# Kernel tuning notes

Measured on AMD Instinct MI355X. Metric: run time of the kernel, lower is better.

The kernel has to match this reference:

```python
import jax, jax.numpy as jnp
import numpy as np

H = 8          # n_heads
EPS = 1e-5     # LayerNorm eps (torch default)


def setup_inputs() -> dict:
    key = jax.random.key(0)
    ks = jax.random.split(key, 16)
    B, N, D, L, C, K = 2, 1000, 6, 12, 32, 16
    dm = L * C  # d_model = 384
    s = 0.02
    inp = {
        "x": jax.random.normal(ks[0], (B, N, D, L, C), dtype=jnp.float32),
        "topk_index": jax.random.randint(ks[1], (B, N, K), 0, N),
        # attention projections (stored as [in, out]; y = x @ W + b)
        "Wq": jax.random.normal(ks[2], (dm, dm), jnp.float32) * s,
        "bq": jnp.zeros((dm,), jnp.float32),
        "Wk": jax.random.normal(ks[3], (dm, dm), jnp.float32) * s,
        "bk": jnp.zeros((dm,), jnp.float32),
        "Wv": jax.random.normal(ks[4], (dm, dm), jnp.float32) * s,
        "bv": jnp.zeros((dm,), jnp.float32),
        "Wo": jax.random.normal(ks[5], (dm, dm), jnp.float32) * s,
        "bo": jnp.zeros((dm,), jnp.float32),
        # LayerNorm over last dim C
        "ln_g": jnp.ones((C,), jnp.float32),
        "ln_b": jnp.zeros((C,), jnp.float32),
        # MLP: C -> 2C -> C with GELU
        "W1": jax.random.normal(ks[6], (C, 2 * C), jnp.float32) * s,
        "b1": jnp.zeros((2 * C,), jnp.float32),
        "W2": jax.random.normal(ks[7], (2 * C, C), jnp.float32) * s,
        "b2": jnp.zeros((C,), jnp.float32),
    }
    return inp


def _forward(x, topk_index, Wq, bq, Wk, bk, Wv, bv, Wo, bo, ln_g, ln_b, W1, b1, W2, b2):
    B, N, D, L, C = x.shape
    dm = L * C
    dk = dm // H

    q = x.reshape(B * N, D, dm)                                   # [BN, D, dm]
    # gather top-k neighbor features: kv[b,i] = x[b, topk_index[b,i]]
    kv = x[jnp.arange(B)[:, None, None], topk_index]              # [B, N, K, D, L, C]
    K_ = topk_index.shape[-1]
    kv = kv.reshape(B * N, K_ * D, dm)                            # [BN, KD, dm]

    Q = (q @ Wq + bq).reshape(B * N, D, H, dk)
    Kp = (kv @ Wk + bk).reshape(B * N, K_ * D, H, dk)
    V = (kv @ Wv + bv).reshape(B * N, K_ * D, H, dk)

    scale = 1.0 / jnp.sqrt(jnp.asarray(dk, x.dtype))
    scores = jnp.einsum('blhe,bshe->bhls', Q, Kp) * scale         # [BN, H, D, KD]
    A = jax.nn.softmax(scores, axis=-1)                           # dropout: eval mode (identity)
    ctx = jnp.einsum('bhls,bshd->blhd', A, V).reshape(B * N, D, dm)
    ctx = (ctx @ Wo + bo).reshape(B, N, D, L, C)

    h = x + ctx                                                   # residual (dropout = identity)
    mu = jnp.mean(h, axis=-1, keepdims=True)
    var = jnp.var(h, axis=-1, keepdims=True)
    fused = (h - mu) / jnp.sqrt(var + EPS) * ln_g + ln_b          # LayerNorm over C

    mlp = jax.nn.gelu(fused @ W1 + b1, approximate=False) @ W2 + b2
    return fused + mlp


def reference(x, topk_index, Wq, bq, Wk, bk, Wv, bv, Wo, bo, ln_g, ln_b, W1, b1, W2, b2):
    return _forward(x, topk_index, Wq, bq, Wk, bk, Wv, bv, Wo, bo, ln_g, ln_b, W1, b1, W2, b2)
```

## Files before the change

### kernel.cpp

```cpp
#include <hip/hip_runtime.h>

#define NB 2
#define NN 1000
#define ND 6
#define NK 16
#define NH 8
#define DM 384
#define MROWS 12000
#define NTOK 2000
#define NS 96

static __device__ __forceinline__ float4 ld4(const float* p){ return *reinterpret_cast<const float4*>(p); }
static __device__ __forceinline__ void st4(float* p, float4 v){ *reinterpret_cast<float4*>(p) = v; }

#define SCALE 0.14433756729740646f
#define GELU_K 0.70710678118654752f

__global__ __launch_bounds__(256, 2)
void k_qkv(const float* __restrict__ x,
           const float* __restrict__ Wq, const float* __restrict__ bq,
           const float* __restrict__ Wk, const float* __restrict__ bk,
           const float* __restrict__ Wv, const float* __restrict__ bv,
           float* __restrict__ Qa, float* __restrict__ Ka, float* __restrict__ Va)
{
    __shared__ float As[16*132];
    __shared__ float Bs[16*128];

    const int tid = threadIdx.x;
    const int tx = tid & 15, ty = tid >> 4;
    const int r0 = blockIdx.x * 128;
    const int wsel = blockIdx.y / 3;
    const int c0 = (blockIdx.y % 3) * 128;
    const float* W   = (wsel == 0) ? Wq : (wsel == 1) ? Wk : Wv;
    const float* bi  = (wsel == 0) ? bq : (wsel == 1) ? bk : bv;
    float*       out = (wsel == 0) ? Qa : (wsel == 1) ? Ka : Va;

    float acc[8][8];
    #pragma unroll
    for (int i = 0; i < 8; i++)
        #pragma unroll
        for (int j = 0; j < 8; j++) acc[i][j] = 0.f;

    const int lrow = tid >> 2;
    const int lkc  = (tid & 3) << 2;
    const int bkr  = tid >> 5;
    const int bcc  = (tid & 31) << 2;

    for (int k0 = 0; k0 < DM; k0 += 16) {
        #pragma unroll
        for (int hf = 0; hf < 2; hf++) {
            const int r = lrow + hf*64;
            const int gr = r0 + r;
            float4 v = make_float4(0.f, 0.f, 0.f, 0.f);
            if (gr < MROWS) v = ld4(&x[(size_t)gr*DM + k0 + lkc]);
            As[(lkc+0)*132 + r] = v.x;
            As[(lkc+1)*132 + r] = v.y;
            As[(lkc+2)*132 + r] = v.z;
            As[(lkc+3)*132 + r] = v.w;
        }
        #pragma unroll
        for (int hf = 0; hf < 2; hf++) {
            const int kr = bkr + hf*8;
            st4(&Bs[kr*128 + bcc], ld4(&W[(size_t)(k0+kr)*DM + c0 + bcc]));
        }
        __syncthreads();
        #pragma unroll
        for (int kk = 0; kk < 16; kk++) {
            const float4 a0 = ld4(&As[kk*132 + 4*ty]);
            const float4 a1 = ld4(&As[kk*132 + 64 + 4*ty]);
            const float4 b0 = ld4(&Bs[kk*128 + 4*tx]);
            const float4 b1 = ld4(&Bs[kk*128 + 64 + 4*tx]);
            const float a[8] = {a0.x,a0.y,a0.z,a0.w,a1.x,a1.y,a1.z,a1.w};
            const float b[8] = {b0.x,b0.y,b0.z,b0.w,b1.x,b1.y,b1.z,b1.w};
            #pragma unroll
            for (int i = 0; i < 8; i++)
                #pragma unroll
                for (int j = 0; j < 8; j++)
                    acc[i][j] = fmaf(a[i], b[j], acc[i][j]);
        }
        __syncthreads();
    }

    #pragma unroll
    for (int i = 0; i < 8; i++) {
        const int r = (i < 4) ? (4*ty + i) : (64 + 4*ty + i - 4);
        const int gr = r0 + r;
        if (gr >= MROWS) continue;
        #pragma unroll
        for (int jh = 0; jh < 2; jh++) {
            const int cl = jh ? (64 + 4*tx) : (4*tx);
            const int c = c0 + cl;
            const float4 bv = ld4(&bi[c]);
            float4 v;
            v.x = acc[i][4*jh+0] + bv.x;
            v.y = acc[i][4*jh+1] + bv.y;
            v.z = acc[i][4*jh+2] + bv.z;
            v.w = acc[i][4*jh+3] + bv.w;
            st4(&out[(size_t)gr*DM + c], v);
        }
    }
}

__global__ __launch_bounds__(256, 3)
void k_attn(float* __restrict__ Qa,
            const float* __restrict__ Ka,
            const float* __restrict__ Va,
            const int* __restrict__ topk)
{
    __shared__ float Qs[6*384];
    __shared__ float Sm[48*98];
    __shared__ float Rs[16*388];
    __shared__ int   idxs[NK];

    const int tid = threadIdx.x;
    const int bn  = blockIdx.x;
    const int bb  = (bn >= NN) ? NN : 0;
    const size_t qbase = (size_t)bn * (ND*DM);

    if (tid < NK) idxs[tid] = topk[bn*NK + tid];
    {
        const float4* src = (const float4*)(Qa + qbase);
        float4* dst = (float4*)Qs;
        #pragma unroll
        for (int p = 0; p < 3; p++) {
            const int i = tid + p*256;
            if (i < 576) dst[i] = src[i];
        }
    }
    __syncthreads();

    const int s_l = tid & 15;
    const int hh8 = (tid >> 4) & 7;
    const int lh  = tid >> 7;

    for (int c = 0; c < 6; ++c) {
        #pragma unroll
        for (int p = 0; p < 6; p++) {
            const int p4 = tid + p*256;
            const int r16 = p4 / 96, c4 = p4 - r16*96;
            const int sg = c*16 + r16;
            const int k = sg / 6, d = sg - k*6;
            const float4 v = ld4(&Ka[((size_t)(bb + idxs[k])*ND + d)*DM + c4*4]);
            st4(&Rs[r16*388 + c4*4], v);
        }
        __syncthreads();
        {
            const float* Krow = &Rs[s_l*388 + hh8*48];
            const float* Q0 = &Qs[(lh*3+0)*384 + hh8*48];
            const float* Q1 = &Qs[(lh*3+1)*384 + hh8*48];
            const float* Q2 = &Qs[(lh*3+2)*384 + hh8*48];
            float a0 = 0.f, a1 = 0.f, a2 = 0.f;
            #pragma unroll
            for (int j = 0; j < 12; ++j) {
                const float4 kv = ld4(&Krow[4*j]);
                const float4 q0 = ld4(&Q0[4*j]);
                const float4 q1 = ld4(&Q1[4*j]);
                const float4 q2 = ld4(&Q2[4*j]);
                a0 = fmaf(kv.x,q0.x, fmaf(kv.y,q0.y, fmaf(kv.z,q0.z, fmaf(kv.w,q0.w, a0))));
                a1 = fmaf(kv.x,q1.x, fmaf(kv.y,q1.y, fmaf(kv.z,q1.z, fmaf(kv.w,q1.w, a1))));
                a2 = fmaf(kv.x,q2.x, fmaf(kv.y,q2.y, fmaf(kv.z,q2.z, fmaf(kv.w,q2.w, a2))));
            }
            const int sg = c*16 + s_l;
            Sm[(hh8*6 + lh*3 + 0)*98 + sg] = a0 * SCALE;
            Sm[(hh8*6 + lh*3 + 1)*98 + sg] = a1 * SCALE;
            Sm[(hh8*6 + lh*3 + 2)*98 + sg] = a2 * SCALE;
        }
        __syncthreads();
    }

    {
        const int g = tid >> 2, l4 = tid & 3;
        if (g < 48) {
            float* row = &Sm[g*98];
            float m = -3.0e38f;
            #pragma unroll
            for (int i = 0; i < 24; ++i) m = fmaxf(m, row[l4 + 4*i]);
            m = fmaxf(m, __shfl_xor(m, 1));
            m = fmaxf(m, __shfl_xor(m, 2));
            float e[24];
            float sum = 0.f;
            #pragma unroll
            for (int i = 0; i < 24; ++i) { e[i] = __expf(row[l4 + 4*i] - m); sum += e[i]; }
            sum += __shfl_xor(sum, 1);
            sum += __shfl_xor(sum, 2);
            const float inv = 1.f / sum;
            #pragma unroll
            for (int i = 0; i < 24; ++i) row[l4 + 4*i] = e[i] * inv;
        }
    }
    __syncthreads();

    const int g  = tid >> 2;
    const int jl = tid & 3;
    const int hh = g / 6, ll = g - hh*6;
    float4 acc0 = make_float4(0.f,0.f,0.f,0.f);
    float4 acc1 = make_float4(0.f,0.f,0.f,0.f);
    float4 acc2 = make_float4(0.f,0.f,0.f,0.f);

    for (int c = 0; c < 6; ++c) {
        #pragma unroll
        for (int p = 0; p < 6; p++) {
            const int p4 = tid + p*256;
            const int r16 = p4 / 96, c4 = p4 - r16*96;
            const int sg = c*16 + r16;
            const int k = sg / 6, d = sg - k*6;
            const float4 v = ld4(&Va[((size_t)(bb + idxs[k])*ND + d)*DM + c4*4]);
            st4(&Rs[r16*388 + c4*4], v);
        }
        __syncthreads();
        if (g < 48) {
            const float* arow = &Sm[g*98 + c*16];
            #pragma unroll
            for (int s = 0; s < 16; ++s) {
                const float a = arow[s];
                const float* vr = &Rs[s*388 + hh*48 + 4*jl];
                const float4 v0 = ld4(&vr[0]);
                const float4 v1 = ld4(&vr[16]);
                const float4 v2 = ld4(&vr[32]);
                acc0.x = fmaf(a, v0.x, acc0.x); acc0.y = fmaf(a, v0.y, acc0.y);
                acc0.z = fmaf(a, v0.z, acc0.z); acc0.w = fmaf(a, v0.w, acc0.w);
                acc1.x = fmaf(a, v1.x, acc1.x); acc1.y = fmaf(a, v1.y, acc1.y);
                acc1.z = fmaf(a, v1.z, acc1.z); acc1.w = fmaf(a, v1.w, acc1.w);
                acc2.x = fmaf(a, v2.x, acc2.x); acc2.y = fmaf(a, v2.y, acc2.y);
                acc2.z = fmaf(a, v2.z, acc2.z); acc2.w = fmaf(a, v2.w, acc2.w);
            }
        }
        __syncthreads();
    }

    if (g < 48) {
        float* dst = &Qa[qbase + (size_t)ll*DM + hh*48 + 4*jl];
        st4(&dst[0],  acc0);
        st4(&dst[16], acc1);
        st4(&dst[32], acc2);
    }
}

__global__ __launch_bounds__(256, 2)
void k_out(const float* __restrict__ ctx, const float* __restrict__ x,
           const float* __restrict__ Wo, const float* __restrict__ bo,
           const float* __restrict__ ln_g, const float* __restrict__ ln_b,
           const float* __restrict__ W1, const float* __restrict__ b1,
           const float* __restrict__ W2, const float* __restrict__ b2,
           float* __restrict__ out)
{
    __shared__ float smem[8256];
    __shared__ float W1s[2048];
    __shared__ float W2t[2048];
    __shared__ float b1s[64];
    __shared__ float cns[96];

    const int tid = threadIdx.x;
    const int tx = tid & 15, ty = tid >> 4;
    const int r0 = blockIdx.x * 64;
    const int c0 = blockIdx.y * 128;

    for (int p = tid; p < 2048; p += 256) {
        W1s[p] = W1[p];
        const int o = p >> 5, c = p & 31;
        W2t[c*64 + o] = W2[p];
    }
    if (tid < 64) b1s[tid] = b1[tid];
    if (tid < 32) { cns[tid] = ln_g[tid]; cns[32+tid] = ln_b[tid]; cns[64+tid] = b2[tid]; }

    float* As = smem;
    float* Bs = smem + 1088;

    float acc[4][8];
    #pragma unroll
    for (int i = 0; i < 4; i++)
        #pragma unroll
        for (int j = 0; j < 8; j++) acc[i][j] = 0.f;

    const int lrow = tid >> 2;
    const int lkc  = (tid & 3) << 2;
    const int bkr  = tid >> 5;
    const int bcc  = (tid & 31) << 2;

    for (int k0 = 0; k0 < DM; k0 += 16) {
        {
            const int gr = r0 + lrow;
            float4 v = make_float4(0.f, 0.f, 0.f, 0.f);
            if (gr < MROWS) v = ld4(&ctx[(size_t)gr*DM + k0 + lkc]);
            As[(lkc+0)*68 + lrow] = v.x;
            As[(lkc+1)*68 + lrow] = v.y;
            As[(lkc+2)*68 + lrow] = v.z;
            As[(lkc+3)*68 + lrow] = v.w;
        }
        #pragma unroll
        for (int hf = 0; hf < 2; hf++) {
            const int kr = bkr + hf*8;
            st4(&Bs[kr*128 + bcc], ld4(&Wo[(size_t)(k0+kr)*DM + c0 + bcc]));
        }
        __syncthreads();
        #pragma unroll
        for (int kk = 0; kk < 16; kk++) {
            const float4 a0 = ld4(&As[kk*68 + 4*ty]);
            const float4 b0 = ld4(&Bs[kk*128 + 4*tx]);
            const float4 b1v = ld4(&Bs[kk*128 + 64 + 4*tx]);
            const float a[4] = {a0.x,a0.y,a0.z,a0.w};
            const float b[8] = {b0.x,b0.y,b0.z,b0.w,b1v.x,b1v.y,b1v.z,b1v.w};
            #pragma unroll
            for (int i = 0; i < 4; i++)
                #pragma unroll
                for (int j = 0; j < 8; j++)
                    acc[i][j] = fmaf(a[i], b[j], acc[i][j]);
        }
        __syncthreads();
    }

    float* hs = smem;
    #pragma unroll
    for (int i = 0; i < 4; i++) {
        const int r = 4*ty + i;
        const int gr = r0 + r;
        if (gr < MROWS) {
            #pragma unroll
            for (int jh = 0; jh < 2; jh++) {
                const int cl = jh ? (64 + 4*tx) : (4*tx);
                const int c = c0 + cl;
                const float4 xv = ld4(&x[(size_t)gr*DM + c]);
                const float4 bv = ld4(&bo[c]);
                hs[r*129 + cl + 0] = acc[i][4*jh+0] + bv.x + xv.x;
                hs[r*129 + cl + 1] = acc[i][4*jh+1] + bv.y + xv.y;
                hs[r*129 + cl + 2] = acc[i][4*jh+2] + bv.z + xv.z;
                hs[r*129 + cl + 3] = acc[i][4*jh+3] + bv.w + xv.w;
            }
        }
    }
    __syncthreads();

    {
        const int row = tid & 63, g = tid >> 6;
        const int gr = r0 + row;
        if (gr < MROWS) {
            const float* hrow = &hs[row*129 + g*32];
            float mu = 0.f;
            #pragma unroll
            for (int c = 0; c < 32; c++) mu += hrow[c];
            mu *= 0.03125f;
            float var = 0.f;
            #pragma unroll
            for (int c = 0; c < 32; c++) { const float d = hrow[c] - mu; var = fmaf(d, d, var); }
            var *= 0.03125f;
            const float rstd = 1.0f / sqrtf(var + 1e-5f);

            float y[64];
            #pragma unroll
            for (int o4 = 0; o4 < 16; o4++) {
                const float4 bv = ld4(&b1s[4*o4]);
                y[4*o4+0] = bv.x; y[4*o4+1] = bv.y; y[4*o4+2] = bv.z; y[4*o4+3] = bv.w;
            }
            for (int c = 0; c < 32; c++) {
                const float fc = (hrow[c] - mu) * rstd * cns[c] + cns[32 + c];
                const float4* w = (const float4*)&W1s[c*64];
                #pragma unroll
                for (int j = 0; j < 16; j++) {
                    const float4 wv = w[j];
                    y[4*j+0] = fmaf(fc, wv.x, y[4*j+0]);
                    y[4*j+1] = fmaf(fc, wv.y, y[4*j+1]);
                    y[4*j+2] = fmaf(fc, wv.z, y[4*j+2]);
                    y[4*j+3] = fmaf(fc, wv.w, y[4*j+3]);
                }
            }
            #pragma unroll
            for (int o = 0; o < 64; o++) {
                const float v = y[o];
                y[o] = 0.5f * v * (1.0f + erff(v * GELU_K));
            }
            float* orow = &out[(size_t)gr*DM + c0 + g*32];
            for (int c = 0; c < 32; c++) {
                const float fc = (hrow[c] - mu) * rstd * cns[c] + cns[32 + c];
                float zc = cns[64 + c];
                const float4* w = (const float4*)&W2t[c*64];
                #pragma unroll
                for (int j = 0; j < 16; j++) {
                    const float4 wv = w[j];
                    zc = fmaf(y[4*j+0], wv.x, zc);
                    zc = fmaf(y[4*j+1], wv.y, zc);
                    zc = fmaf(y[4*j+2], wv.z, zc);
                    zc = fmaf(y[4*j+3], wv.w, zc);
                }
                orow[c] = fc + zc;
            }
        }
    }
}

extern "C" void kernel_launch(void* const* d_in, const int* in_sizes, int n_in,
                              void* d_out, int out_size, void* d_ws, size_t ws_size,
                              hipStream_t stream)
{
    const float* x   = (const float*)d_in[0];
    const int*   tk  = (const int*)  d_in[1];
    const float* Wq  = (const float*)d_in[2];
    const float* bq  = (const float*)d_in[3];
    const float* Wk  = (const float*)d_in[4];
    const float* bk  = (const float*)d_in[5];
    const float* Wv  = (const float*)d_in[6];
    const float* bv  = (const float*)d_in[7];
    const float* Wo  = (const float*)d_in[8];
    const float* bo  = (const float*)d_in[9];
    const float* lng = (const float*)d_in[10];
    const float* lnb = (const float*)d_in[11];
    const float* W1  = (const float*)d_in[12];
    const float* b1  = (const float*)d_in[13];
    const float* W2  = (const float*)d_in[14];
    const float* b2  = (const float*)d_in[15];
    float* out = (float*)d_out;

    float* Qa = (float*)d_ws;
    float* Ka = Qa + (size_t)MROWS * DM;
    float* Va = Ka + (size_t)MROWS * DM;

    k_qkv<<<dim3(94, 9), 256, 0, stream>>>(x, Wq, bq, Wk, bk, Wv, bv, Qa, Ka, Va);
    k_attn<<<dim3(NTOK), 256, 0, stream>>>(Qa, Ka, Va, tk);
    k_out<<<dim3(188, 3), 256, 0, stream>>>(Qa, x, Wo, bo, lng, lnb, W1, b1, W2, b2, out);
}
```

Measured before the change: 450.7 us.

## Compute QKV projection with split-bf16 MFMA instead of FP32 FMA

Adds a conversion kernel that splits x and the Q/K/V weights into high and low bf16 halves, storing the weights transposed. The QKV GEMM then uses MFMA 16x16x32 bf16 instructions with three products (hi*hi, lo*hi, hi*lo) to approximate FP32 precision. The aim is to move the projection GEMM from scalar FP32 FMAs onto the matrix cores. In exchange it adds an extra pass over x and extra workspace, and accuracy is slightly below true FP32.

```diff
diff --git a/kernel.cpp b/kernel.cpp
--- a/kernel.cpp
+++ b/kernel.cpp
@@ -10,93 +10,150 @@
 #define NTOK 2000
 #define NS 96
 
+typedef unsigned short u16;
+typedef __attribute__((ext_vector_type(8))) short bf16x8;
+typedef __attribute__((ext_vector_type(4))) float f32x4;
+
 static __device__ __forceinline__ float4 ld4(const float* p){ return *reinterpret_cast<const float4*>(p); }
 static __device__ __forceinline__ void st4(float* p, float4 v){ *reinterpret_cast<float4*>(p) = v; }
 
 #define SCALE 0.14433756729740646f
 #define GELU_K 0.70710678118654752f
 
+static __device__ __forceinline__ u16 bf_hi(float a){
+    unsigned u = __float_as_uint(a);
+    unsigned r = u + 0x7fffu + ((u >> 16) & 1u);
+    return (u16)(r >> 16);
+}
+static __device__ __forceinline__ void bf_split(float a, u16& h, u16& l){
+    h = bf_hi(a);
+    const float hf = __uint_as_float(((unsigned)h) << 16);
+    l = bf_hi(a - hf);
+}
+
+#define NX4 1152000
+#define NW4 36864
+__global__ __launch_bounds__(256)
+void k_convert(const float* __restrict__ x,
+               const float* __restrict__ Wq, const float* __restrict__ Wk,
+               const float* __restrict__ Wv,
+               u16* __restrict__ xh, u16* __restrict__ xl,
+               u16* __restrict__ Wth, u16* __restrict__ Wtl)
+{
+    const int idx = blockIdx.x * 256 + threadIdx.x;
+    if (idx < NX4) {
+        const float4 v = ld4(&x[(size_t)idx*4]);
+        u16 h0,l0,h1,l1,h2,l2,h3,l3;
+        bf_split(v.x,h0,l0); bf_split(v.y,h1,l1); bf_split(v.z,h2,l2); bf_split(v.w,h3,l3);
+        ushort4 vh; vh.x=h0; vh.y=h1; vh.z=h2; vh.w=h3;
+        ushort4 vl; vl.x=l0; vl.y=l1; vl.z=l2; vl.w=l3;
+        *reinterpret_cast<ushort4*>(&xh[(size_t)idx*4]) = vh;
+        *reinterpret_cast<ushort4*>(&xl[(size_t)idx*4]) = vl;
+    } else if (idx < NX4 + 3*NW4) {
+        int t = idx - NX4;
+        const int w = t / NW4; t -= w*NW4;
+        const float* W = (w==0) ? Wq : (w==1) ? Wk : Wv;
+        const int k  = t / 96;
+        const int n4 = (t - k*96) * 4;
+        const float4 v = ld4(&W[(size_t)k*DM + n4]);
+        u16* oh = Wth + (size_t)w*DM*DM;
+        u16* ol = Wtl + (size_t)w*DM*DM;
+        u16 h,l;
+        bf_split(v.x,h,l); oh[(size_t)(n4+0)*DM + k] = h; ol[(size_t)(n4+0)*DM + k] = l;
+        bf_split(v.y,h,l); oh[(size_t)(n4+1)*DM + k] = h; ol[(size_t)(n4+1)*DM + k] = l;
+        bf_split(v.z,h,l); oh[(size_t)(n4+2)*DM + k] = h; ol[(size_t)(n4+2)*DM + k] = l;
+        bf_split(v.w,h,l); oh[(size_t)(n4+3)*DM + k] = h; ol[(size_t)(n4+3)*DM + k] = l;
+    }
+}
+
 __global__ __launch_bounds__(256, 2)
-void k_qkv(const float* __restrict__ x,
-           const float* __restrict__ Wq, const float* __restrict__ bq,
-           const float* __restrict__ Wk, const float* __restrict__ bk,
-           const float* __restrict__ Wv, const float* __restrict__ bv,
-           float* __restrict__ Qa, float* __restrict__ Ka, float* __restrict__ Va)
+void k_qkvm(const u16* __restrict__ xh, const u16* __restrict__ xl,
+            const u16* __restrict__ Wth, const u16* __restrict__ Wtl,
+            const float* __restrict__ bq, const float* __restrict__ bk,
+            const float* __restrict__ bv,
+            float* __restrict__ Qa, float* __restrict__ Ka, float* __restrict__ Va)
 {
-    __shared__ float As[16*132];
-    __shared__ float Bs[16*128];
+    __shared__ u16 Ash[2][8192];
+    __shared__ u16 Bsh[2][8192];
 
     const int tid = threadIdx.x;
-    const int tx = tid & 15, ty = tid >> 4;
     const int r0 = blockIdx.x * 128;
     const int wsel = blockIdx.y / 3;
     const int c0 = (blockIdx.y % 3) * 128;
-    const float* W   = (wsel == 0) ? Wq : (wsel == 1) ? Wk : Wv;
-    const float* bi  = (wsel == 0) ? bq : (wsel == 1) ? bk : bv;
-    float*       out = (wsel == 0) ? Qa : (wsel == 1) ? Ka : Va;
-
-    float acc[8][8];
+    const u16* Wh = Wth + (size_t)wsel * DM * DM;
+    const u16* Wl = Wtl + (size_t)wsel * DM * DM;
+
+    const int lane = tid & 63, wid = tid >> 6;
+    const int wm = wid >> 1, wn = wid & 1;
+    const int fr = lane & 15, fg = lane >> 4;
+
+    f32x4 acc[4][4];
     #pragma unroll
-    for (int i = 0; i < 8; i++)
-        #pragma unroll
-        for (int j = 0; j < 8; j++) acc[i][j] = 0.f;
-
-    const int lrow = tid >> 2;
-    const int lkc  = (tid & 3) << 2;
-    const int bkr  = tid >> 5;
-    const int bcc  = (tid & 31) << 2;
-
-    for (int k0 = 0; k0 < DM; k0 += 16) {
-        #pragma unroll
-        for (int hf = 0; hf < 2; hf++) {
-            const int r = lrow + hf*64;
-            const int gr = r0 + r;
-            float4 v = make_float4(0.f, 0.f, 0.f, 0.f);
-            if (gr < MROWS) v = ld4(&x[(size_t)gr*DM + k0 + lkc]);
-            As[(lkc+0)*132 + r] = v.x;
-            As[(lkc+1)*132 + r] = v.y;
-            As[(lkc+2)*132 + r] = v.z;
-            As[(lkc+3)*132 + r] = v.w;
-        }
-        #pragma unroll
-        for (int hf = 0; hf < 2; hf++) {
-            const int kr = bkr + hf*8;
-            st4(&Bs[kr*128 + bcc], ld4(&W[(size_t)(k0+kr)*DM + c0 + bcc]));
-        }
-        __syncthreads();
-        #pragma unroll
-        for (int kk = 0; kk < 16; kk++) {
-            const float4 a0 = ld4(&As[kk*132 + 4*ty]);
-            const float4 a1 = ld4(&As[kk*132 + 64 + 4*ty]);
-            const float4 b0 = ld4(&Bs[kk*128 + 4*tx]);
-            const float4 b1 = ld4(&Bs[kk*128 + 64 + 4*tx]);
-            const float a[8] = {a0.x,a0.y,a0.z,a0.w,a1.x,a1.y,a1.z,a1.w};
-            const float b[8] = {b0.x,b0.y,b0.z,b0.w,b1.x,b1.y,b1.z,b1.w};
-            #pragma unroll
-            for (int i = 0; i < 8; i++)
+    for (int i = 0; i < 4; i++)
+        #pragma unroll
+        for (int j = 0; j < 4; j++) acc[i][j] = (f32x4){0.f,0.f,0.f,0.f};
+
+    const int srow = tid >> 3;
+    const int skc  = tid & 7;
+
+    for (int k0 = 0; k0 < DM; k0 += 64) {
+        __syncthreads();
+        #pragma unroll
+        for (int p = 0; p < 4; ++p) {
+            const int row = srow + p*32;
+            const int lo = skc*1024 + row*8;
+            const int gr = r0 + row;
+            uint4 vh = make_uint4(0u,0u,0u,0u), vl = vh;
+            if (gr < MROWS) {
+                const size_t ga = (size_t)gr*DM + k0 + skc*8;
+                vh = *reinterpret_cast<const uint4*>(&xh[ga]);
+                vl = *reinterpret_cast<const uint4*>(&xl[ga]);
+            }
+            *reinterpret_cast<uint4*>(&Ash[0][lo]) = vh;
+            *reinterpret_cast<uint4*>(&Ash[1][lo]) = vl;
+            const size_t gb = (size_t)(c0 + row)*DM + k0 + skc*8;
+            *reinterpret_cast<uint4*>(&Bsh[0][lo]) = *reinterpret_cast<const uint4*>(&Wh[gb]);
+            *reinterpret_cast<uint4*>(&Bsh[1][lo]) = *reinterpret_cast<const uint4*>(&Wl[gb]);
+        }
+        __syncthreads();
+        #pragma unroll
+        for (int ks = 0; ks < 2; ++ks) {
+            const int kb = (ks*4 + fg) * 1024;
+            bf16x8 ah[4], al[4], bh[4], blo[4];
+            #pragma unroll
+            for (int t = 0; t < 4; ++t) {
+                const int ro = kb + (wm*64 + t*16 + fr)*8;
+                ah[t] = *reinterpret_cast<const bf16x8*>(&Ash[0][ro]);
+                al[t] = *reinterpret_cast<const bf16x8*>(&Ash[1][ro]);
+                const int co = kb + (wn*64 + t*16 + fr)*8;
+                bh[t]  = *reinterpret_cast<const bf16x8*>(&Bsh[0][co]);
+                blo[t] = *reinterpret_cast<const bf16x8*>(&Bsh[1][co]);
+            }
+            #pragma unroll
+            for (int mt = 0; mt < 4; ++mt)
                 #pragma unroll
-                for (int j = 0; j < 8; j++)
-                    acc[i][j] = fmaf(a[i], b[j], acc[i][j]);
-        }
-        __syncthreads();
-    }
-
+                for (int nt = 0; nt < 4; ++nt) {
+                    acc[mt][nt] = __builtin_amdgcn_mfma_f32_16x16x32_bf16(ah[mt], bh[nt],  acc[mt][nt], 0,0,0);
+                    acc[mt][nt] = __builtin_amdgcn_mfma_f32_16x16x32_bf16(al[mt], bh[nt],  acc[mt][nt], 0,0,0);
+                    acc[mt][nt] = __builtin_amdgcn_mfma_f32_16x16x32_bf16(ah[mt], blo[nt], acc[mt][nt], 0,0,0);
+                }
+        }
+    }
+
+    const float* bias = (wsel==0) ? bq : (wsel==1) ? bk : bv;
+    float*       outp = (wsel==0) ? Qa : (wsel==1) ? Ka : Va;
     #pragma unroll
-    for (int i = 0; i < 8; i++) {
-        const int r = (i < 4) ? (4*ty + i) : (64 + 4*ty + i - 4);
-        const int gr = r0 + r;
-        if (gr >= MROWS) continue;
-        #pragma unroll
-        for (int jh = 0; jh < 2; jh++) {
-            const int cl = jh ? (64 + 4*tx) : (4*tx);
-            const int c = c0 + cl;
-            const float4 bv = ld4(&bi[c]);
-            float4 v;
-            v.x = acc[i][4*jh+0] + bv.x;
-            v.y = acc[i][4*jh+1] + bv.y;
-            v.z = acc[i][4*jh+2] + bv.z;
-            v.w = acc[i][4*jh+3] + bv.w;
-            st4(&out[(size_t)gr*DM + c], v);
+    for (int mt = 0; mt < 4; ++mt) {
+        const int rbase = r0 + wm*64 + mt*16 + fg*4;
+        #pragma unroll
+        for (int nt = 0; nt < 4; ++nt) {
+            const int col = c0 + wn*64 + nt*16 + fr;
+            const float bb_ = bias[col];
+            #pragma unroll
+            for (int i = 0; i < 4; ++i) {
+                const int rr = rbase + i;
+                if (rr < MROWS) outp[(size_t)rr*DM + col] = acc[mt][nt][i] + bb_;
+            }
         }
     }
 }
@@ -412,8 +469,13 @@
     float* Qa = (float*)d_ws;
     float* Ka = Qa + (size_t)MROWS * DM;
     float* Va = Ka + (size_t)MROWS * DM;
-
-    k_qkv<<<dim3(94, 9), 256, 0, stream>>>(x, Wq, bq, Wk, bk, Wv, bv, Qa, Ka, Va);
+    u16* xh  = (u16*)(Va + (size_t)MROWS * DM);
+    u16* xl  = xh + (size_t)MROWS * DM;
+    u16* Wth = xl + (size_t)MROWS * DM;
+    u16* Wtl = Wth + (size_t)3 * DM * DM;
+
+    k_convert<<<dim3(4932), 256, 0, stream>>>(x, Wq, Wk, Wv, xh, xl, Wth, Wtl);
+    k_qkvm<<<dim3(94, 9), 256, 0, stream>>>(xh, xl, Wth, Wtl, bq, bk, bv, Qa, Ka, Va);
     k_attn<<<dim3(NTOK), 256, 0, stream>>>(Qa, Ka, Va, tk);
     k_out<<<dim3(188, 3), 256, 0, stream>>>(Qa, x, Wo, bo, lng, lnb, W1, b1, W2, b2, out);
 }
```

Result: faster. 391.3 us (-13.2%).
